# Kernel optimization log

Hardware: AMD Instinct MI355X
Metric: run time of the kernel (lower is better)

## Reference

```python
import jax, jax.numpy as jnp
import numpy as np

B, H, W, A, C = 8, 13, 13, 5, 20
ANCHORS = [[1.3221, 1.73145], [3.19275, 4.00944], [5.05587, 8.09892],
           [9.47112, 4.84053], [11.2364, 10.0071]]
L_COORD, OBJ_SCALE, NOOBJ_SCALE = 3.0, 5.0, 1.0
POS_FRAC_THRESH = 0.98


def gen_yolo_box():
    # anchor[..., 0:2] = (x_col, y_row) grid offsets, anchor[..., 2:4] = anchor (w, h)
    ys, xs = jnp.meshgrid(jnp.arange(H, dtype=jnp.float32),
                          jnp.arange(W, dtype=jnp.float32), indexing='ij')
    grid = jnp.broadcast_to(jnp.stack([xs, ys], -1)[:, :, None, :], (H, W, A, 2))
    wh = jnp.broadcast_to(jnp.asarray(ANCHORS, jnp.float32)[None, None], (H, W, A, 2))
    return jnp.concatenate([grid, wh], -1)  # [H, W, A, 4]


def decode(delta, anc, fs0, fs1):
    # delta: [..., 4] raw offsets; anc: [..., 4]; returns [x1, y1, w, h]
    w = jnp.exp(delta[..., 2]) * anc[..., 2] / fs0
    h = jnp.exp(delta[..., 3]) * anc[..., 3] / fs1
    x = (delta[..., 0] + anc[..., 0]) / fs0 - w * 0.5
    y = (delta[..., 1] + anc[..., 1]) / fs1 - h * 0.5
    return jnp.stack([x, y, w, h], -1)


def pairwise_iou(b1, b2):
    # b1: [N,4], b2: [M,4] in [x1,y1,w,h]; returns [N, M]
    b1x1, b1y1 = b1[:, 0:1], b1[:, 1:2]
    b1x2, b1y2 = b1x1 + b1[:, 2:3], b1y1 + b1[:, 3:4]
    b2x1, b2y1, b2x2, b2y2 = b2[:, 0], b2[:, 1], b2[:, 0] + b2[:, 2], b2[:, 1] + b2[:, 3]
    dx = jnp.clip(jnp.minimum(b1x2, b2x2[None, :]) - jnp.maximum(b1x1, b2x1[None, :]), 0)
    dy = jnp.clip(jnp.minimum(b1y2, b2y2[None, :]) - jnp.maximum(b1y1, b2y1[None, :]), 0)
    inter = dx * dy
    a1 = (b1x2 - b1x1) * (b1y2 - b1y1)          # [N,1]
    a2 = (b2x2 - b2x1) * (b2y2 - b2y1)          # [M]
    return inter / (a1 + a2[None, :] - inter)


def elem_iou(b1, b2):
    # elementwise IoU over [..., 4] boxes ([x1,y1,w,h])
    b1x2, b1y2 = b1[..., 0] + b1[..., 2], b1[..., 1] + b1[..., 3]
    b2x2, b2y2 = b2[..., 0] + b2[..., 2], b2[..., 1] + b2[..., 3]
    dx = jnp.clip(jnp.minimum(b1x2, b2x2) - jnp.maximum(b1[..., 0], b2[..., 0]), 0)
    dy = jnp.clip(jnp.minimum(b1y2, b2y2) - jnp.maximum(b1[..., 1], b2[..., 1]), 0)
    inter = dx * dy
    a1 = b1[..., 2] * b1[..., 3]
    a2 = b2[..., 2] * b2[..., 3]
    return inter / (a1 + a2 - inter)


def setup_inputs() -> dict:
    key = jax.random.key(0)
    ks = jax.random.split(key, 6)
    pred_cls = jax.random.normal(ks[0], (B, H, W, A, C), jnp.float32)
    pred_conf = jax.random.uniform(ks[1], (B, H, W, A, 1), jnp.float32)
    pred_bboxes = jax.random.normal(ks[2], (B, H, W, A, 4), jnp.float32)
    label_cls = jax.random.normal(ks[3], (B, H, W, A, C), jnp.float32)
    u = jax.random.uniform(ks[4], (B, H, W, A, 1), jnp.float32)
    label_conf = (u > POS_FRAC_THRESH).astype(jnp.float32)  # sparse positives
    label_bboxes = jax.random.uniform(ks[5], (B, H, W, A, 4), jnp.float32)
    return {"pred_cls": pred_cls, "pred_conf": pred_conf, "pred_bboxes": pred_bboxes,
            "label_cls": label_cls, "label_conf": label_conf, "label_bboxes": label_bboxes}


def reference(pred_cls, pred_conf, pred_bboxes, label_cls, label_conf, label_bboxes):
    dt = pred_bboxes.dtype
    fs0, fs1 = float(H), float(W)
    pos = label_conf[..., 0] > 0                 # [B,H,W,A]
    posf = pos.astype(dt)
    anc = gen_yolo_box()[None]                   # [1,H,W,A,4]

    gt_box = decode(label_bboxes, anc, fs0, fs1)   # [B,H,W,A,4]
    pred_box = decode(pred_bboxes, anc, fs0, fs1)  # [B,H,W,A,4]

    # "diagonal" IoU: each positive gt paired with the pred box at the same cell
    diag_iou = elem_iou(gt_box, pred_box)          # [B,H,W,A]
    p_conf = pred_conf[..., 0]
    loss_pos_conf = jnp.sum(posf * (p_conf - jax.lax.stop_gradient(diag_iou)) ** 2) \
        * OBJ_SCALE / B

    # dense masked pairwise IoU (gt rows masked to 0 where not positive)
    N = B * H * W * A
    iou_mat = pairwise_iou(gt_box.reshape(N, 4), pred_box.reshape(N, 4))  # [N,N]
    pos_flat = pos.reshape(N)
    iou_mat = jnp.where(pos_flat[:, None], iou_mat, jnp.zeros((), dt))
    best = jnp.max(iou_mat, axis=0)                       # per pred box
    best = jnp.where(pos_flat, jnp.ones((), dt), best)    # ious_[pos] = 1
    negf = (best < 0.6).astype(dt)
    loss_neg_conf = jnp.sum(negf * (p_conf.reshape(N) - label_conf.reshape(N)) ** 2) \
        * NOOBJ_SCALE / B

    # classification CE (sum) over positives
    logp = jax.nn.log_softmax(pred_cls, axis=-1)
    lbl = jnp.argmax(label_cls, axis=-1)
    nll = -jnp.take_along_axis(logp, lbl[..., None], axis=-1)[..., 0]
    loss_cls = jnp.sum(posf * nll) / B

    # coordinate losses over positives
    dxy = pred_bboxes[..., :2] - label_bboxes[..., :2]
    loss_x = jnp.sum(posf * dxy[..., 0] ** 2) * L_COORD / B
    loss_y = jnp.sum(posf * dxy[..., 1] ** 2) * L_COORD / B

    def huber(d):  # SmoothL1, beta=1
        ad = jnp.abs(d)
        return jnp.where(ad < 1.0, 0.5 * d * d, ad - 0.5)

    dwh = pred_bboxes[..., 2:4] - label_bboxes[..., 2:4]
    loss_w = jnp.sum(posf * huber(dwh[..., 0])) * L_COORD / B
    loss_h = jnp.sum(posf * huber(dwh[..., 1])) * L_COORD / B

    return loss_x + loss_y + loss_w + loss_h + loss_cls + loss_neg_conf + loss_pos_conf
```

## Files before the change

kernel.cpp:

```cpp
#include <hip/hip_runtime.h>

#define NB 8
#define HH 13
#define WW 13
#define AA 5
#define CC 20
#define NTOT (NB * HH * WW * AA)
#define L_COORD 3.0f
#define OBJ_SCALE 5.0f
#define INV_B (1.0f / 8.0f)
#define FS 13.0f
#define BLOCK 256
#define GRID ((NTOT + BLOCK - 1) / BLOCK)
#define SEG BLOCK
#define SCAP 3584

#define WS_BOX_OFFSET 1024

__device__ __constant__ float c_anc[AA][2] = {
    {1.3221f, 1.73145f}, {3.19275f, 4.00944f}, {5.05587f, 8.09892f},
    {9.47112f, 4.84053f}, {11.2364f, 10.0071f}};

__device__ __forceinline__ float block_reduce_sum(float v, float* sbuf) {
    for (int o = 32; o > 0; o >>= 1) v += __shfl_down(v, o);
    if ((threadIdx.x & 63) == 0) sbuf[threadIdx.x >> 6] = v;
    __syncthreads();
    float s = 0.f;
    if (threadIdx.x == 0) {
        for (int i = 0; i < (BLOCK >> 6); i++) s += sbuf[i];
    }
    return s;
}

__global__ void __launch_bounds__(BLOCK) yolo_k1(
    const float* __restrict__ pred_cls,
    const float* __restrict__ pred_conf,
    const float4* __restrict__ pred_bboxes,
    const float* __restrict__ label_cls,
    const float* __restrict__ label_conf,
    const float4* __restrict__ label_bboxes,
    float* __restrict__ out,
    int* __restrict__ cnt_ws,
    float4* __restrict__ box_ws) {
    __shared__ int s_c;
    __shared__ float sred[BLOCK >> 6];

    const int tid = threadIdx.x;
    const int n   = blockIdx.x * BLOCK + tid;
    if (tid == 0) s_c = 0;
    __syncthreads();

    float local = 0.f;
    if (n < NTOT) {
        float lcf = label_conf[n];
        if (lcf > 0.f) {
            int a = n % AA;
            int w = (n / AA) % WW;
            int h = (n / (AA * WW)) % HH;
            float ancw = c_anc[a][0], anch = c_anc[a][1];

            float4 pb = pred_bboxes[n];
            float4 tb = label_bboxes[n];
            float  pc = pred_conf[n];

            float pw = expf(pb.z) * ancw * (1.f / FS);
            float ph = expf(pb.w) * anch * (1.f / FS);
            float px1 = (pb.x + (float)w) * (1.f / FS) - pw * 0.5f;
            float py1 = (pb.y + (float)h) * (1.f / FS) - ph * 0.5f;
            float px2 = px1 + pw, py2 = py1 + ph;

            float gw = expf(tb.z) * ancw * (1.f / FS);
            float gh = expf(tb.w) * anch * (1.f / FS);
            float gx = (tb.x + (float)w) * (1.f / FS) - gw * 0.5f;
            float gy = (tb.y + (float)h) * (1.f / FS) - gh * 0.5f;
            float gx2 = gx + gw, gy2 = gy + gh;

            float dx = fminf(gx2, px2) - fmaxf(gx, px1); dx = fmaxf(dx, 0.f);
            float dy = fminf(gy2, py2) - fmaxf(gy, py1); dy = fmaxf(dy, 0.f);
            float inter = dx * dy;
            float iou = inter / (gw * gh + pw * ph - inter);
            float dconf = pc - iou;
            local += OBJ_SCALE * dconf * dconf;

            const float4* lc4 = reinterpret_cast<const float4*>(label_cls) + (long)n * 5;
            const float4* pc4 = reinterpret_cast<const float4*>(pred_cls) + (long)n * 5;
            float lrow[CC], prow[CC];
            #pragma unroll
            for (int q = 0; q < 5; q++) {
                float4 v = lc4[q];
                lrow[4 * q + 0] = v.x; lrow[4 * q + 1] = v.y;
                lrow[4 * q + 2] = v.z; lrow[4 * q + 3] = v.w;
                float4 u = pc4[q];
                prow[4 * q + 0] = u.x; prow[4 * q + 1] = u.y;
                prow[4 * q + 2] = u.z; prow[4 * q + 3] = u.w;
            }
            int lbl = 0;
            float bl = lrow[0];
            #pragma unroll
            for (int i = 1; i < CC; i++)
                if (lrow[i] > bl) { bl = lrow[i]; lbl = i; }
            float mx = prow[0];
            #pragma unroll
            for (int i = 1; i < CC; i++) mx = fmaxf(mx, prow[i]);
            float s = 0.f;
            #pragma unroll
            for (int i = 0; i < CC; i++) s += expf(prow[i] - mx);
            local += mx + logf(s) - prow[lbl];

            float dxc = pb.x - tb.x, dyc = pb.y - tb.y;
            local += L_COORD * (dxc * dxc + dyc * dyc);
            float dwc = pb.z - tb.z, dhc = pb.w - tb.w;
            float adw = fabsf(dwc), adh = fabsf(dhc);
            float hw  = adw < 1.f ? 0.5f * dwc * dwc : adw - 0.5f;
            float hh2 = adh < 1.f ? 0.5f * dhc * dhc : adh - 0.5f;
            local += L_COORD * (hw + hh2);

            int idx = atomicAdd(&s_c, 1);
            box_ws[blockIdx.x * SEG + idx] = make_float4(gx, gy, gx2, gy2);
        }
    }
    __syncthreads();
    if (tid == 0) cnt_ws[blockIdx.x] = s_c;

    float bs = block_reduce_sum(local, sred);
    if (tid == 0) atomicAdd(out, bs * INV_B);
}

__global__ void __launch_bounds__(BLOCK) yolo_k2(
    const float* __restrict__ pred_conf,
    const float4* __restrict__ pred_bboxes,
    const float* __restrict__ label_conf,
    float* __restrict__ out,
    const int* __restrict__ cnt_ws,
    const float4* __restrict__ box_ws) {
    __shared__ float4 sbox[SCAP];
    __shared__ int scnt[32];
    __shared__ float sred[BLOCK >> 6];

    const int tid = threadIdx.x;
    const int n   = blockIdx.x * BLOCK + tid;

    bool  neg = false;
    float px1 = 0.f, py1 = 0.f, px2 = 0.f, py2 = 0.f, parea = 1.f, diffsq = 0.f;
    if (n < NTOT) {
        float lcf = label_conf[n];
        if (!(lcf > 0.f)) {
            neg = true;
            int a = n % AA;
            int w = (n / AA) % WW;
            int h = (n / (AA * WW)) % HH;
            float4 pb = pred_bboxes[n];
            float pw = expf(pb.z) * c_anc[a][0] * (1.f / FS);
            float ph = expf(pb.w) * c_anc[a][1] * (1.f / FS);
            px1 = (pb.x + (float)w) * (1.f / FS) - pw * 0.5f;
            py1 = (pb.y + (float)h) * (1.f / FS) - ph * 0.5f;
            px2 = px1 + pw;
            py2 = py1 + ph;
            parea = pw * ph;
            float d = pred_conf[n] - lcf;
            diffsq = d * d;
        }
    }

    if (tid < GRID) scnt[tid] = cnt_ws[tid];
    __syncthreads();

    int Mtot = 0;
    #pragma unroll
    for (int b = 0; b < GRID; b++) Mtot += scnt[b];

    float best = 0.f;
    if (Mtot <= SCAP) {
        int off = 0;
        #pragma unroll
        for (int b = 0; b < GRID; b++) {
            int cb = scnt[b];
            if (tid < cb) sbox[off + tid] = box_ws[b * SEG + tid];
            off += cb;
        }
        __syncthreads();
        if (neg) {
            #pragma unroll 4
            for (int i = 0; i < Mtot; i++) {
                float4 g = sbox[i];
                float dx = fminf(px2, g.z) - fmaxf(px1, g.x); dx = fmaxf(dx, 0.f);
                float dy = fminf(py2, g.w) - fmaxf(py1, g.y); dy = fmaxf(dy, 0.f);
                float inter = dx * dy;
                float garea = (g.z - g.x) * (g.w - g.y);
                float iou = inter / (garea + parea - inter);
                best = fmaxf(best, iou);
            }
        }
        __syncthreads();
    } else {
        if (neg) {
            for (int b = 0; b < GRID; b++) {
                int cb = scnt[b];
                for (int i = 0; i < cb; i++) {
                    float4 g = box_ws[b * SEG + i];
                    float dx = fminf(px2, g.z) - fmaxf(px1, g.x); dx = fmaxf(dx, 0.f);
                    float dy = fminf(py2, g.w) - fmaxf(py1, g.y); dy = fmaxf(dy, 0.f);
                    float inter = dx * dy;
                    float garea = (g.z - g.x) * (g.w - g.y);
                    float iou = inter / (garea + parea - inter);
                    best = fmaxf(best, iou);
                }
            }
        }
    }

    float contrib = (neg && best < 0.6f) ? diffsq : 0.f;
    float bs = block_reduce_sum(contrib, sred);
    if (tid == 0) atomicAdd(out, bs * INV_B);
}

extern "C" void kernel_launch(void* const* d_in, const int* in_sizes, int n_in,
                              void* d_out, int out_size, void* d_ws, size_t ws_size,
                              hipStream_t stream) {
    const float*  pred_cls     = (const float*)d_in[0];
    const float*  pred_conf    = (const float*)d_in[1];
    const float4* pred_bboxes  = (const float4*)d_in[2];
    const float*  label_cls    = (const float*)d_in[3];
    const float*  label_conf   = (const float*)d_in[4];
    const float4* label_bboxes = (const float4*)d_in[5];
    float* out = (float*)d_out;

    int*    cnt_ws = (int*)d_ws;
    float4* box_ws = (float4*)((char*)d_ws + WS_BOX_OFFSET);

    yolo_k1<<<GRID, BLOCK, 0, stream>>>(
        pred_cls, pred_conf, pred_bboxes, label_cls, label_conf, label_bboxes,
        out, cnt_ws, box_ws);
    yolo_k2<<<GRID, BLOCK, 0, stream>>>(
        pred_conf, pred_bboxes, label_conf, out, cnt_ws, box_ws);
}
```

Before: 95.82 us.

## Fuse two loss kernels into one cooperative kernel with grid sync

Merges the positive-cell kernel and the negative-cell IoU kernel into a single cooperative launch, using a grid-wide sync in place of the kernel boundary so the predicted box is decoded once and kept in registers. It also replaces the per-pair IoU division with a division-free test (inter > 0.375*(ga+pa), which is equivalent to IoU >= 0.6). The aim is to remove one launch and its gap, plus the divides in the inner loop. The cost is cooperative-launch overhead and a grid barrier, and every block now holds the large shared box buffer even while doing positive work.

```diff
diff --git a/kernel.cpp b/kernel.cpp
--- a/kernel.cpp
+++ b/kernel.cpp
@@ -1,4 +1,7 @@
 #include <hip/hip_runtime.h>
+#include <hip/hip_cooperative_groups.h>
+
+namespace cg = cooperative_groups;
 
 #define NB 8
 #define HH 13
@@ -32,7 +35,7 @@
     return s;
 }
 
-__global__ void __launch_bounds__(BLOCK) yolo_k1(
+__global__ void __launch_bounds__(BLOCK) yolo_coop_kernel(
     const float* __restrict__ pred_cls,
     const float* __restrict__ pred_conf,
     const float4* __restrict__ pred_bboxes,
@@ -42,7 +45,9 @@
     float* __restrict__ out,
     int* __restrict__ cnt_ws,
     float4* __restrict__ box_ws) {
+    __shared__ float4 sbox[SCAP];
     __shared__ int s_c;
+    __shared__ int scnt[32];
     __shared__ float sred[BLOCK >> 6];
 
     const int tid = threadIdx.x;
@@ -51,24 +56,30 @@
     __syncthreads();
 
     float local = 0.f;
+    bool  neg = false;
+    float px1 = 0.f, py1 = 0.f, px2 = 0.f, py2 = 0.f, parea38 = 0.f, diffsq = 0.f;
+
     if (n < NTOT) {
-        float lcf = label_conf[n];
+        int a = n % AA;
+        int w = (n / AA) % WW;
+        int h = (n / (AA * WW)) % HH;
+        float ancw = c_anc[a][0], anch = c_anc[a][1];
+
+        float4 pb  = pred_bboxes[n];
+        float  lcf = label_conf[n];
+        float  pc  = pred_conf[n];
+
+        float pw = expf(pb.z) * ancw * (1.f / FS);
+        float ph = expf(pb.w) * anch * (1.f / FS);
+        px1 = (pb.x + (float)w) * (1.f / FS) - pw * 0.5f;
+        py1 = (pb.y + (float)h) * (1.f / FS) - ph * 0.5f;
+        px2 = px1 + pw;
+        py2 = py1 + ph;
+        float parea = pw * ph;
+        parea38 = 0.375f * parea;
+
         if (lcf > 0.f) {
-            int a = n % AA;
-            int w = (n / AA) % WW;
-            int h = (n / (AA * WW)) % HH;
-            float ancw = c_anc[a][0], anch = c_anc[a][1];
-
-            float4 pb = pred_bboxes[n];
             float4 tb = label_bboxes[n];
-            float  pc = pred_conf[n];
-
-            float pw = expf(pb.z) * ancw * (1.f / FS);
-            float ph = expf(pb.w) * anch * (1.f / FS);
-            float px1 = (pb.x + (float)w) * (1.f / FS) - pw * 0.5f;
-            float py1 = (pb.y + (float)h) * (1.f / FS) - ph * 0.5f;
-            float px2 = px1 + pw, py2 = py1 + ph;
-
             float gw = expf(tb.z) * ancw * (1.f / FS);
             float gh = expf(tb.w) * anch * (1.f / FS);
             float gx = (tb.x + (float)w) * (1.f / FS) - gw * 0.5f;
@@ -78,7 +89,7 @@
             float dx = fminf(gx2, px2) - fmaxf(gx, px1); dx = fmaxf(dx, 0.f);
             float dy = fminf(gy2, py2) - fmaxf(gy, py1); dy = fmaxf(dy, 0.f);
             float inter = dx * dy;
-            float iou = inter / (gw * gh + pw * ph - inter);
+            float iou = inter / (gw * gh + parea - inter);
             float dconf = pc - iou;
             local += OBJ_SCALE * dconf * dconf;
 
@@ -117,50 +128,17 @@
 
             int idx = atomicAdd(&s_c, 1);
             box_ws[blockIdx.x * SEG + idx] = make_float4(gx, gy, gx2, gy2);
+        } else {
+            neg = true;
+            float d = pc - lcf;
+            diffsq = d * d;
         }
     }
     __syncthreads();
     if (tid == 0) cnt_ws[blockIdx.x] = s_c;
 
-    float bs = block_reduce_sum(local, sred);
-    if (tid == 0) atomicAdd(out, bs * INV_B);
-}
-
-__global__ void __launch_bounds__(BLOCK) yolo_k2(
-    const float* __restrict__ pred_conf,
-    const float4* __restrict__ pred_bboxes,
-    const float* __restrict__ label_conf,
-    float* __restrict__ out,
-    const int* __restrict__ cnt_ws,
-    const float4* __restrict__ box_ws) {
-    __shared__ float4 sbox[SCAP];
-    __shared__ int scnt[32];
-    __shared__ float sred[BLOCK >> 6];
-
-    const int tid = threadIdx.x;
-    const int n   = blockIdx.x * BLOCK + tid;
-
-    bool  neg = false;
-    float px1 = 0.f, py1 = 0.f, px2 = 0.f, py2 = 0.f, parea = 1.f, diffsq = 0.f;
-    if (n < NTOT) {
-        float lcf = label_conf[n];
-        if (!(lcf > 0.f)) {
-            neg = true;
-            int a = n % AA;
-            int w = (n / AA) % WW;
-            int h = (n / (AA * WW)) % HH;
-            float4 pb = pred_bboxes[n];
-            float pw = expf(pb.z) * c_anc[a][0] * (1.f / FS);
-            float ph = expf(pb.w) * c_anc[a][1] * (1.f / FS);
-            px1 = (pb.x + (float)w) * (1.f / FS) - pw * 0.5f;
-            py1 = (pb.y + (float)h) * (1.f / FS) - ph * 0.5f;
-            px2 = px1 + pw;
-            py2 = py1 + ph;
-            parea = pw * ph;
-            float d = pred_conf[n] - lcf;
-            diffsq = d * d;
-        }
-    }
+    __threadfence();
+    cg::this_grid().sync();
 
     if (tid < GRID) scnt[tid] = cnt_ws[tid];
     __syncthreads();
@@ -169,7 +147,7 @@
     #pragma unroll
     for (int b = 0; b < GRID; b++) Mtot += scnt[b];
 
-    float best = 0.f;
+    float viol = -1.f;
     if (Mtot <= SCAP) {
         int off = 0;
         #pragma unroll
@@ -186,12 +164,10 @@
                 float dx = fminf(px2, g.z) - fmaxf(px1, g.x); dx = fmaxf(dx, 0.f);
                 float dy = fminf(py2, g.w) - fmaxf(py1, g.y); dy = fmaxf(dy, 0.f);
                 float inter = dx * dy;
-                float garea = (g.z - g.x) * (g.w - g.y);
-                float iou = inter / (garea + parea - inter);
-                best = fmaxf(best, iou);
+                float ga38 = 0.375f * ((g.z - g.x) * (g.w - g.y));
+                viol = fmaxf(viol, inter - (ga38 + parea38));
             }
         }
-        __syncthreads();
     } else {
         if (neg) {
             for (int b = 0; b < GRID; b++) {
@@ -201,16 +177,17 @@
                     float dx = fminf(px2, g.z) - fmaxf(px1, g.x); dx = fmaxf(dx, 0.f);
                     float dy = fminf(py2, g.w) - fmaxf(py1, g.y); dy = fmaxf(dy, 0.f);
                     float inter = dx * dy;
-                    float garea = (g.z - g.x) * (g.w - g.y);
-                    float iou = inter / (garea + parea - inter);
-                    best = fmaxf(best, iou);
+                    float ga38 = 0.375f * ((g.z - g.x) * (g.w - g.y));
+                    viol = fmaxf(viol, inter - (ga38 + parea38));
                 }
             }
         }
+        __syncthreads();
     }
 
-    float contrib = (neg && best < 0.6f) ? diffsq : 0.f;
-    float bs = block_reduce_sum(contrib, sred);
+    if (neg && viol < 0.f) local += diffsq;
+
+    float bs = block_reduce_sum(local, sred);
     if (tid == 0) atomicAdd(out, bs * INV_B);
 }
 
@@ -228,9 +205,11 @@
     int*    cnt_ws = (int*)d_ws;
     float4* box_ws = (float4*)((char*)d_ws + WS_BOX_OFFSET);
 
-    yolo_k1<<<GRID, BLOCK, 0, stream>>>(
-        pred_cls, pred_conf, pred_bboxes, label_cls, label_conf, label_bboxes,
-        out, cnt_ws, box_ws);
-    yolo_k2<<<GRID, BLOCK, 0, stream>>>(
-        pred_conf, pred_bboxes, label_conf, out, cnt_ws, box_ws);
+    void* args[] = {
+        (void*)&pred_cls, (void*)&pred_conf, (void*)&pred_bboxes,
+        (void*)&label_cls, (void*)&label_conf, (void*)&label_bboxes,
+        (void*)&out, (void*)&cnt_ws, (void*)&box_ws};
+
+    hipLaunchCooperativeKernel((const void*)yolo_coop_kernel,
+                               dim3(GRID), dim3(BLOCK), args, 0, stream);
 }
```

Result: slower. 119.1 us (+24.3%).
